# Kernel tuning notes

Measured on AMD Instinct MI355X. Metric: run time of the kernel, lower is better.

The kernel has to match this reference:

```python
import jax, jax.numpy as jnp
import numpy as np

N_NODES = 50000
N_EDGES = 800000
D_NODE = 64
D_EDGE = 64
MSG_DIM = 64           # n_features_list_messages[-1]
MLP_FEATS = [128, 128, 64]  # n_features_list_nodes
LN_EPS = 1e-6


def setup_inputs() -> dict:
    key = jax.random.key(0)
    ks = jax.random.split(key, 16)
    nodes = jax.random.normal(ks[0], (N_NODES, D_NODE), dtype=jnp.float32)
    edges = jax.random.normal(ks[1], (N_EDGES, D_EDGE), dtype=jnp.float32)
    senders = jax.random.randint(ks[2], (N_EDGES,), 0, N_NODES, dtype=jnp.int32)
    receivers = jax.random.randint(ks[3], (N_EDGES,), 0, N_NODES, dtype=jnp.int32)

    def glorot(k, shape):
        fan_in, fan_out = shape[0], shape[1]
        s = jnp.sqrt(2.0 / (fan_in + fan_out))
        return jax.random.normal(k, shape, dtype=jnp.float32) * s

    W_message = glorot(ks[4], (D_NODE + D_EDGE, MSG_DIM))      # no bias
    W_node = glorot(ks[5], (D_NODE, MLP_FEATS[-1]))            # no bias
    mlp_in_dim = D_NODE + MSG_DIM
    mlp_w0 = glorot(ks[6], (mlp_in_dim, MLP_FEATS[0]))
    mlp_b0 = jnp.zeros((MLP_FEATS[0],), dtype=jnp.float32)
    mlp_w1 = glorot(ks[7], (MLP_FEATS[0], MLP_FEATS[1]))
    mlp_b1 = jnp.zeros((MLP_FEATS[1],), dtype=jnp.float32)
    mlp_w2 = glorot(ks[8], (MLP_FEATS[1], MLP_FEATS[2]))
    mlp_b2 = jnp.zeros((MLP_FEATS[2],), dtype=jnp.float32)
    ln_scale = jnp.ones((MLP_FEATS[-1],), dtype=jnp.float32)
    ln_bias = jnp.zeros((MLP_FEATS[-1],), dtype=jnp.float32)

    return {
        "nodes": nodes, "edges": edges, "senders": senders, "receivers": receivers,
        "W_message": W_message, "W_node": W_node,
        "mlp_w0": mlp_w0, "mlp_b0": mlp_b0,
        "mlp_w1": mlp_w1, "mlp_b1": mlp_b1,
        "mlp_w2": mlp_w2, "mlp_b2": mlp_b2,
        "ln_scale": ln_scale, "ln_bias": ln_bias,
    }


def reference(nodes, edges, senders, receivers, W_message, W_node,
              mlp_w0, mlp_b0, mlp_w1, mlp_b1, mlp_w2, mlp_b2,
              ln_scale, ln_bias):
    # gather sender node features [E, d_node]
    sender_features = nodes[senders]
    # linear message on concat(sender, edge) [E, msg_dim]
    msg_in = jnp.concatenate([sender_features, edges], axis=-1)
    messages = msg_in @ W_message
    # scatter-add into receiver buckets [N, msg_dim]
    aggregated = jax.ops.segment_sum(messages, receivers, num_segments=N_NODES)
    # node MLP with ReLU hidden layers, linear output
    h = jnp.concatenate([nodes, aggregated], axis=-1)
    h = jax.nn.relu(h @ mlp_w0 + mlp_b0)
    h = jax.nn.relu(h @ mlp_w1 + mlp_b1)
    nodes_out = h @ mlp_w2 + mlp_b2
    # residual (linear skip) + LayerNorm
    x = nodes @ W_node + nodes_out
    mu = jnp.mean(x, axis=-1, keepdims=True)
    var = jnp.var(x, axis=-1, keepdims=True)
    nodes_new = (x - mu) * jax.lax.rsqrt(var + LN_EPS) * ln_scale + ln_bias
    return nodes_new
```

## Files before the change

### kernel.cpp

```cpp
#include <hip/hip_runtime.h>
#include <cstdint>
#include <cstddef>


__global__ void hist_k(const int* __restrict__ recv, int* __restrict__ hist, int E){
  int i = blockIdx.x*blockDim.x + threadIdx.x;
  if (i < E) atomicAdd(&hist[recv[i]], 1);
}

__global__ void s1_k(const int* __restrict__ hist, int* __restrict__ partial, int Nn){
  __shared__ int sh[256];
  int t = threadIdx.x;
  int i = blockIdx.x*256 + t;
  sh[t] = (i < Nn) ? hist[i] : 0;
  __syncthreads();
  for (int off = 128; off > 0; off >>= 1){
    if (t < off) sh[t] += sh[t + off];
    __syncthreads();
  }
  if (t == 0) partial[blockIdx.x] = sh[0];
}

__global__ void s2_k(int* __restrict__ partial, int nb){
  int lane = threadIdx.x;
  int run = 0;
  for (int base = 0; base < nb; base += 64){
    int v = (base + lane < nb) ? partial[base + lane] : 0;
    int x = v;
    #pragma unroll
    for (int off = 1; off < 64; off <<= 1){
      int y = __shfl_up(x, off);
      if (lane >= off) x += y;
    }
    if (base + lane < nb) partial[base + lane] = x - v + run;
    run += __shfl(x, 63);
  }
}

__global__ void s3_k(const int* __restrict__ hist, const int* __restrict__ partial,
                     int* __restrict__ offsets, int* __restrict__ cursor, int Nn){
  __shared__ int sh[256];
  int t = threadIdx.x;
  int i = blockIdx.x*256 + t;
  int v = (i < Nn) ? hist[i] : 0;
  sh[t] = v;
  __syncthreads();
  for (int off = 1; off < 256; off <<= 1){
    int x = (t >= off) ? sh[t - off] : 0;
    __syncthreads();
    sh[t] += x;
    __syncthreads();
  }
  if (i < Nn){
    int excl = sh[t] - v + partial[blockIdx.x];
    offsets[i] = excl;
    cursor[i]  = excl;
  }
}

__global__ void fill_k(const int* __restrict__ recv, const int* __restrict__ senders,
                       int* __restrict__ cursor, int2* __restrict__ csr_pack, int E){
  int i = blockIdx.x*blockDim.x + threadIdx.x;
  if (i < E){
    int r = recv[i];
    int s = senders[i];
    int pos = atomicAdd(&cursor[r], 1);
    csr_pack[pos] = make_int2(i, s);
  }
}

__global__ __launch_bounds__(256) void gather_sum_k(
    const float* __restrict__ nodes, const float* __restrict__ edges,
    const int2* __restrict__ csr_pack, const int* __restrict__ offsets,
    const int* __restrict__ hist, float* __restrict__ SE, int Nn)
{
  int wid  = threadIdx.x >> 6;
  int lane = threadIdx.x & 63;
  int node = blockIdx.x*4 + wid;
  if (node >= Nn) return;
  int start = offsets[node];
  int cnt   = hist[node];
  float sa = 0.f, ea = 0.f;
  int done = 0;
  while (done < cnt){
    int m = cnt - done; if (m > 64) m = 64;
    int2 pk = make_int2(0, 0);
    if (lane < m) pk = csr_pack[start + done + lane];
    int u = 0;
    for (; u + 4 <= m; u += 4){
      int e0 = __shfl(pk.x, u+0), s0 = __shfl(pk.y, u+0);
      int e1 = __shfl(pk.x, u+1), s1 = __shfl(pk.y, u+1);
      int e2 = __shfl(pk.x, u+2), s2 = __shfl(pk.y, u+2);
      int e3 = __shfl(pk.x, u+3), s3 = __shfl(pk.y, u+3);
      float n0 = nodes[(size_t)s0*64 + lane];
      float n1 = nodes[(size_t)s1*64 + lane];
      float n2 = nodes[(size_t)s2*64 + lane];
      float n3 = nodes[(size_t)s3*64 + lane];
      float g0 = edges[(size_t)e0*64 + lane];
      float g1 = edges[(size_t)e1*64 + lane];
      float g2 = edges[(size_t)e2*64 + lane];
      float g3 = edges[(size_t)e3*64 + lane];
      sa += (n0 + n1) + (n2 + n3);
      ea += (g0 + g1) + (g2 + g3);
    }
    for (; u < m; u++){
      int e0 = __shfl(pk.x, u), s0 = __shfl(pk.y, u);
      sa += nodes[(size_t)s0*64 + lane];
      ea += edges[(size_t)e0*64 + lane];
    }
    done += m;
  }
  SE[(size_t)node*128 + lane]      = sa;
  SE[(size_t)node*128 + 64 + lane] = ea;
}

__global__ void transpose_k(const float* __restrict__ in, float* __restrict__ out, int R, int C){
  __shared__ float tile[32][33];
  int c0 = blockIdx.x*32, r0 = blockIdx.y*32;
  int tx = threadIdx.x, ty = threadIdx.y;
  #pragma unroll
  for (int i = 0; i < 32; i += 8){
    int r = r0 + ty + i, c = c0 + tx;
    if (r < R && c < C) tile[ty + i][tx] = in[(size_t)r*C + c];
  }
  __syncthreads();
  #pragma unroll
  for (int i = 0; i < 32; i += 8){
    int c = c0 + ty + i, r = r0 + tx;
    if (r < R && c < C) out[(size_t)c*R + r] = tile[tx][ty + i];
  }
}

__global__ void wprep_k(const float* __restrict__ Wmsg, const float* __restrict__ w0,
                        const float* __restrict__ w2, const float* __restrict__ Wnode,
                        float* __restrict__ W1eff, float* __restrict__ W3eff){
  int idx = blockIdx.x*blockDim.x + threadIdx.x;
  if (idx < 192*128){
    int r = idx >> 7, j = idx & 127;
    float v;
    if (r < 64) v = w0[r*128 + j];
    else {
      int kk = r - 64;
      float a = 0.f;
      for (int m = 0; m < 64; m++) a = fmaf(Wmsg[kk*64 + m], w0[(64 + m)*128 + j], a);
      v = a;
    }
    W1eff[idx] = v;
  }
  if (idx < 192*64){
    int r = idx >> 6, j = idx & 63;
    W3eff[idx] = (r < 128) ? w2[r*64 + j] : Wnode[(r - 128)*64 + j];
  }
}


__global__ __launch_bounds__(256) void layer1_k(
    const float* __restrict__ nodesT, const float* __restrict__ SET,
    const float* __restrict__ W, const float* __restrict__ bias,
    float* __restrict__ outT, int N)
{
  int n  = blockIdx.x*256 + threadIdx.x;
  int jb = blockIdx.y*64;
  if (n >= N) return;
  float acc[64];
  #pragma unroll
  for (int j = 0; j < 64; j++) acc[j] = bias[jb + j];
  for (int k = 0; k < 64; k++){
    float x = nodesT[(size_t)k*N + n];
    #pragma unroll
    for (int j = 0; j < 64; j++) acc[j] = fmaf(x, W[k*128 + jb + j], acc[j]);
  }
  for (int k = 0; k < 128; k++){
    float x = SET[(size_t)k*N + n];
    #pragma unroll
    for (int j = 0; j < 64; j++) acc[j] = fmaf(x, W[(64 + k)*128 + jb + j], acc[j]);
  }
  #pragma unroll
  for (int j = 0; j < 64; j++) outT[(size_t)(jb + j)*N + n] = fmaxf(acc[j], 0.f);
}

__global__ __launch_bounds__(256) void layer2_k(
    const float* __restrict__ inT, const float* __restrict__ W, const float* __restrict__ bias,
    float* __restrict__ outT, int N)
{
  int n  = blockIdx.x*256 + threadIdx.x;
  int jb = blockIdx.y*64;
  if (n >= N) return;
  float acc[64];
  #pragma unroll
  for (int j = 0; j < 64; j++) acc[j] = bias[jb + j];
  for (int k = 0; k < 128; k++){
    float x = inT[(size_t)k*N + n];
    #pragma unroll
    for (int j = 0; j < 64; j++) acc[j] = fmaf(x, W[k*128 + jb + j], acc[j]);
  }
  #pragma unroll
  for (int j = 0; j < 64; j++) outT[(size_t)(jb + j)*N + n] = fmaxf(acc[j], 0.f);
}

__global__ __launch_bounds__(256) void layer3_k(
    const float* __restrict__ X2T, const float* __restrict__ nodesT,
    const float* __restrict__ W, const float* __restrict__ bias,
    const float* __restrict__ ln_scale, const float* __restrict__ ln_bias,
    float* __restrict__ out, int N)
{
  int n = blockIdx.x*256 + threadIdx.x;
  if (n >= N) return;
  float acc[64];
  #pragma unroll
  for (int j = 0; j < 64; j++) acc[j] = bias[j];
  for (int k = 0; k < 128; k++){
    float x = X2T[(size_t)k*N + n];
    #pragma unroll
    for (int j = 0; j < 64; j++) acc[j] = fmaf(x, W[k*64 + j], acc[j]);
  }
  for (int k = 0; k < 64; k++){
    float x = nodesT[(size_t)k*N + n];
    #pragma unroll
    for (int j = 0; j < 64; j++) acc[j] = fmaf(x, W[(128 + k)*64 + j], acc[j]);
  }
  float mu = 0.f;
  #pragma unroll
  for (int j = 0; j < 64; j++) mu += acc[j];
  mu *= (1.f/64.f);
  float var = 0.f;
  #pragma unroll
  for (int j = 0; j < 64; j++){ float d = acc[j] - mu; var = fmaf(d, d, var); }
  var *= (1.f/64.f);
  float inv = rsqrtf(var + 1e-6f);
  float4* o = (float4*)(out + (size_t)n*64);
  #pragma unroll
  for (int q = 0; q < 16; q++){
    float y0 = (acc[4*q+0] - mu)*inv*ln_scale[4*q+0] + ln_bias[4*q+0];
    float y1 = (acc[4*q+1] - mu)*inv*ln_scale[4*q+1] + ln_bias[4*q+1];
    float y2 = (acc[4*q+2] - mu)*inv*ln_scale[4*q+2] + ln_bias[4*q+2];
    float y3 = (acc[4*q+3] - mu)*inv*ln_scale[4*q+3] + ln_bias[4*q+3];
    o[q] = make_float4(y0, y1, y2, y3);
  }
}


extern "C" void kernel_launch(void* const* d_in, const int* in_sizes, int n_in,
                              void* d_out, int out_size, void* d_ws, size_t ws_size,
                              hipStream_t stream)
{
  const float* nodes   = (const float*)d_in[0];
  const float* edges   = (const float*)d_in[1];
  const int*   senders = (const int*)d_in[2];
  const int*   recv    = (const int*)d_in[3];
  const float* Wmsg    = (const float*)d_in[4];
  const float* Wnode   = (const float*)d_in[5];
  const float* w0      = (const float*)d_in[6];
  const float* b0      = (const float*)d_in[7];
  const float* w1      = (const float*)d_in[8];
  const float* b1      = (const float*)d_in[9];
  const float* w2      = (const float*)d_in[10];
  const float* b2      = (const float*)d_in[11];
  const float* lns     = (const float*)d_in[12];
  const float* lnb     = (const float*)d_in[13];
  float* out = (float*)d_out;

  const int N = in_sizes[0] / 64;
  const int E = in_sizes[2];

  auto align256 = [](size_t x){ return (x + 255) & ~(size_t)255; };
  char* p = (char*)d_ws;
  int* hist    = (int*)p; p += align256((size_t)N*4);
  int* offsets = (int*)p; p += align256((size_t)N*4);
  int* cursor  = (int*)p; p += align256((size_t)N*4);
  int* partial = (int*)p; p += align256(1024);
  int2* csr_pack = (int2*)p; p += align256((size_t)E*8);
  float* W1eff = (float*)p; p += align256((size_t)192*128*4);
  float* W3eff = (float*)p; p += align256((size_t)192*64*4);
  float* nodesT= (float*)p; p += align256((size_t)64*N*4);
  float* bufA  = (float*)p; p += align256((size_t)128*N*4);
  float* bufB  = (float*)p; p += align256((size_t)128*N*4);

  hipMemsetAsync(hist, 0, (size_t)N*4, stream);

  const int gridE = (E + 255)/256;
  const int nb    = (N + 255)/256;

  hist_k<<<gridE, 256, 0, stream>>>(recv, hist, E);
  s1_k<<<nb, 256, 0, stream>>>(hist, partial, N);
  s2_k<<<1, 64, 0, stream>>>(partial, nb);
  s3_k<<<nb, 256, 0, stream>>>(hist, partial, offsets, cursor, N);
  fill_k<<<gridE, 256, 0, stream>>>(recv, senders, cursor, csr_pack, E);

  gather_sum_k<<<(N + 3)/4, 256, 0, stream>>>(nodes, edges, csr_pack, offsets, hist, bufA, N);

  dim3 tb(32, 8);
  transpose_k<<<dim3(2, (N + 31)/32), tb, 0, stream>>>(nodes, nodesT, N, 64);
  transpose_k<<<dim3(4, (N + 31)/32), tb, 0, stream>>>(bufA, bufB, N, 128);

  wprep_k<<<(192*128 + 255)/256, 256, 0, stream>>>(Wmsg, w0, w2, Wnode, W1eff, W3eff);

  layer1_k<<<dim3(nb, 2), 256, 0, stream>>>(nodesT, bufB, W1eff, b0, bufA, N);
  layer2_k<<<dim3(nb, 2), 256, 0, stream>>>(bufA, w1, b1, bufB, N);
  layer3_k<<<nb, 256, 0, stream>>>(bufB, nodesT, W3eff, b2, lns, lnb, out, N);
}
```

Before: 644.4 us.

## Fuse transpose into gather, merge weight prep into scan, narrow MLP column tiles

Measured after the change: 673.6 us. 1.05x slower.

```diff
diff --git a/kernel.cpp b/kernel.cpp
--- a/kernel.cpp
+++ b/kernel.cpp
@@ -8,7 +8,10 @@
   if (i < E) atomicAdd(&hist[recv[i]], 1);
 }
 
-__global__ void s1_k(const int* __restrict__ hist, int* __restrict__ partial, int Nn){
+__global__ void s1_k(const int* __restrict__ hist, int* __restrict__ partial, int Nn,
+                     const float* __restrict__ Wmsg, const float* __restrict__ w0,
+                     const float* __restrict__ w2, const float* __restrict__ Wnode,
+                     float* __restrict__ W1eff, float* __restrict__ W3eff){
   __shared__ int sh[256];
   int t = threadIdx.x;
   int i = blockIdx.x*256 + t;
@@ -19,6 +22,24 @@
     __syncthreads();
   }
   if (t == 0) partial[blockIdx.x] = sh[0];
+
+  int idx = blockIdx.x*256 + t;
+  if (idx < 192*128){
+    int r = idx >> 7, j = idx & 127;
+    float v;
+    if (r < 64) v = w0[r*128 + j];
+    else {
+      int kk = r - 64;
+      float a = 0.f;
+      for (int m = 0; m < 64; m++) a = fmaf(Wmsg[kk*64 + m], w0[(64 + m)*128 + j], a);
+      v = a;
+    }
+    W1eff[idx] = v;
+  }
+  if (idx < 192*64){
+    int r = idx >> 6, j = idx & 63;
+    W3eff[idx] = (r < 128) ? w2[r*64 + j] : Wnode[(r - 128)*64 + j];
+  }
 }
 
 __global__ void s2_k(int* __restrict__ partial, int nb){
@@ -72,111 +93,97 @@
 __global__ __launch_bounds__(256) void gather_sum_k(
     const float* __restrict__ nodes, const float* __restrict__ edges,
     const int2* __restrict__ csr_pack, const int* __restrict__ offsets,
-    const int* __restrict__ hist, float* __restrict__ SE, int Nn)
-{
+    const int* __restrict__ hist, float* __restrict__ XT, int Nn)
+{
+  __shared__ float tile[128][65];
   int wid  = threadIdx.x >> 6;
   int lane = threadIdx.x & 63;
-  int node = blockIdx.x*4 + wid;
-  if (node >= Nn) return;
-  int start = offsets[node];
-  int cnt   = hist[node];
-  float sa = 0.f, ea = 0.f;
-  int done = 0;
-  while (done < cnt){
-    int m = cnt - done; if (m > 64) m = 64;
-    int2 pk = make_int2(0, 0);
-    if (lane < m) pk = csr_pack[start + done + lane];
-    int u = 0;
-    for (; u + 4 <= m; u += 4){
-      int e0 = __shfl(pk.x, u+0), s0 = __shfl(pk.y, u+0);
-      int e1 = __shfl(pk.x, u+1), s1 = __shfl(pk.y, u+1);
-      int e2 = __shfl(pk.x, u+2), s2 = __shfl(pk.y, u+2);
-      int e3 = __shfl(pk.x, u+3), s3 = __shfl(pk.y, u+3);
-      float n0 = nodes[(size_t)s0*64 + lane];
-      float n1 = nodes[(size_t)s1*64 + lane];
-      float n2 = nodes[(size_t)s2*64 + lane];
-      float n3 = nodes[(size_t)s3*64 + lane];
-      float g0 = edges[(size_t)e0*64 + lane];
-      float g1 = edges[(size_t)e1*64 + lane];
-      float g2 = edges[(size_t)e2*64 + lane];
-      float g3 = edges[(size_t)e3*64 + lane];
-      sa += (n0 + n1) + (n2 + n3);
-      ea += (g0 + g1) + (g2 + g3);
+  int nblock = blockIdx.x * 64;
+
+  for (int it = 0; it < 16; ++it){
+    int nd = nblock + wid*16 + it;
+    float sa = 0.f, ea = 0.f;
+    if (nd < Nn){
+      int start = offsets[nd];
+      int cnt   = hist[nd];
+      int done = 0;
+      while (done < cnt){
+        int m = cnt - done; if (m > 64) m = 64;
+        int2 pk = make_int2(0, 0);
+        if (lane < m) pk = csr_pack[start + done + lane];
+        int u = 0;
+        for (; u + 4 <= m; u += 4){
+          int e0 = __shfl(pk.x, u+0), s0 = __shfl(pk.y, u+0);
+          int e1 = __shfl(pk.x, u+1), s1 = __shfl(pk.y, u+1);
+          int e2 = __shfl(pk.x, u+2), s2 = __shfl(pk.y, u+2);
+          int e3 = __shfl(pk.x, u+3), s3 = __shfl(pk.y, u+3);
+          float n0 = nodes[(size_t)s0*64 + lane];
+          float n1 = nodes[(size_t)s1*64 + lane];
+          float n2 = nodes[(size_t)s2*64 + lane];
+          float n3 = nodes[(size_t)s3*64 + lane];
+          float g0 = edges[(size_t)e0*64 + lane];
+          float g1 = edges[(size_t)e1*64 + lane];
+          float g2 = edges[(size_t)e2*64 + lane];
+          float g3 = edges[(size_t)e3*64 + lane];
+          sa += (n0 + n1) + (n2 + n3);
+          ea += (g0 + g1) + (g2 + g3);
+        }
+        for (; u < m; u++){
+          int e0 = __shfl(pk.x, u), s0 = __shfl(pk.y, u);
+          sa += nodes[(size_t)s0*64 + lane];
+          ea += edges[(size_t)e0*64 + lane];
+        }
+        done += m;
+      }
     }
-    for (; u < m; u++){
-      int e0 = __shfl(pk.x, u), s0 = __shfl(pk.y, u);
-      sa += nodes[(size_t)s0*64 + lane];
-      ea += edges[(size_t)e0*64 + lane];
-    }
-    done += m;
-  }
-  SE[(size_t)node*128 + lane]      = sa;
-  SE[(size_t)node*128 + 64 + lane] = ea;
+    int c = wid*16 + it;
+    tile[lane][c]      = sa;
+    tile[64 + lane][c] = ea;
+  }
+  __syncthreads();
+
+  for (int r4 = 0; r4 < 128; r4 += 4){
+    int r = r4 + wid;
+    int n = nblock + lane;
+    if (n < Nn) XT[(size_t)(64 + r)*Nn + n] = tile[r][lane];
+  }
 }
 
 __global__ void transpose_k(const float* __restrict__ in, float* __restrict__ out, int R, int C){
-  __shared__ float tile[32][33];
+  __shared__ float tl[32][33];
   int c0 = blockIdx.x*32, r0 = blockIdx.y*32;
   int tx = threadIdx.x, ty = threadIdx.y;
   #pragma unroll
   for (int i = 0; i < 32; i += 8){
     int r = r0 + ty + i, c = c0 + tx;
-    if (r < R && c < C) tile[ty + i][tx] = in[(size_t)r*C + c];
+    if (r < R && c < C) tl[ty + i][tx] = in[(size_t)r*C + c];
   }
   __syncthreads();
   #pragma unroll
   for (int i = 0; i < 32; i += 8){
     int c = c0 + ty + i, r = r0 + tx;
-    if (r < R && c < C) out[(size_t)c*R + r] = tile[tx][ty + i];
-  }
-}
-
-__global__ void wprep_k(const float* __restrict__ Wmsg, const float* __restrict__ w0,
-                        const float* __restrict__ w2, const float* __restrict__ Wnode,
-                        float* __restrict__ W1eff, float* __restrict__ W3eff){
-  int idx = blockIdx.x*blockDim.x + threadIdx.x;
-  if (idx < 192*128){
-    int r = idx >> 7, j = idx & 127;
-    float v;
-    if (r < 64) v = w0[r*128 + j];
-    else {
-      int kk = r - 64;
-      float a = 0.f;
-      for (int m = 0; m < 64; m++) a = fmaf(Wmsg[kk*64 + m], w0[(64 + m)*128 + j], a);
-      v = a;
-    }
-    W1eff[idx] = v;
-  }
-  if (idx < 192*64){
-    int r = idx >> 6, j = idx & 63;
-    W3eff[idx] = (r < 128) ? w2[r*64 + j] : Wnode[(r - 128)*64 + j];
+    if (r < R && c < C) out[(size_t)c*R + r] = tl[tx][ty + i];
   }
 }
 
 
 __global__ __launch_bounds__(256) void layer1_k(
-    const float* __restrict__ nodesT, const float* __restrict__ SET,
-    const float* __restrict__ W, const float* __restrict__ bias,
+    const float* __restrict__ XT, const float* __restrict__ W, const float* __restrict__ bias,
     float* __restrict__ outT, int N)
 {
   int n  = blockIdx.x*256 + threadIdx.x;
-  int jb = blockIdx.y*64;
+  int jb = blockIdx.y*32;
   if (n >= N) return;
-  float acc[64];
-  #pragma unroll
-  for (int j = 0; j < 64; j++) acc[j] = bias[jb + j];
-  for (int k = 0; k < 64; k++){
-    float x = nodesT[(size_t)k*N + n];
-    #pragma unroll
-    for (int j = 0; j < 64; j++) acc[j] = fmaf(x, W[k*128 + jb + j], acc[j]);
-  }
-  for (int k = 0; k < 128; k++){
-    float x = SET[(size_t)k*N + n];
-    #pragma unroll
-    for (int j = 0; j < 64; j++) acc[j] = fmaf(x, W[(64 + k)*128 + jb + j], acc[j]);
-  }
-  #pragma unroll
-  for (int j = 0; j < 64; j++) outT[(size_t)(jb + j)*N + n] = fmaxf(acc[j], 0.f);
+  float acc[32];
+  #pragma unroll
+  for (int j = 0; j < 32; j++) acc[j] = bias[jb + j];
+  for (int k = 0; k < 192; k++){
+    float x = XT[(size_t)k*N + n];
+    #pragma unroll
+    for (int j = 0; j < 32; j++) acc[j] = fmaf(x, W[k*128 + jb + j], acc[j]);
+  }
+  #pragma unroll
+  for (int j = 0; j < 32; j++) outT[(size_t)(jb + j)*N + n] = fmaxf(acc[j], 0.f);
 }
 
 __global__ __launch_bounds__(256) void layer2_k(
@@ -184,18 +191,18 @@
     float* __restrict__ outT, int N)
 {
   int n  = blockIdx.x*256 + threadIdx.x;
-  int jb = blockIdx.y*64;
+  int jb = blockIdx.y*32;
   if (n >= N) return;
-  float acc[64];
-  #pragma unroll
-  for (int j = 0; j < 64; j++) acc[j] = bias[jb + j];
+  float acc[32];
+  #pragma unroll
+  for (int j = 0; j < 32; j++) acc[j] = bias[jb + j];
   for (int k = 0; k < 128; k++){
     float x = inT[(size_t)k*N + n];
     #pragma unroll
-    for (int j = 0; j < 64; j++) acc[j] = fmaf(x, W[k*128 + jb + j], acc[j]);
-  }
-  #pragma unroll
-  for (int j = 0; j < 64; j++) outT[(size_t)(jb + j)*N + n] = fmaxf(acc[j], 0.f);
+    for (int j = 0; j < 32; j++) acc[j] = fmaf(x, W[k*128 + jb + j], acc[j]);
+  }
+  #pragma unroll
+  for (int j = 0; j < 32; j++) outT[(size_t)(jb + j)*N + n] = fmaxf(acc[j], 0.f);
 }
 
 __global__ __launch_bounds__(256) void layer3_k(
@@ -272,7 +279,7 @@
   int2* csr_pack = (int2*)p; p += align256((size_t)E*8);
   float* W1eff = (float*)p; p += align256((size_t)192*128*4);
   float* W3eff = (float*)p; p += align256((size_t)192*64*4);
-  float* nodesT= (float*)p; p += align256((size_t)64*N*4);
+  float* XT    = (float*)p; p += align256((size_t)192*N*4);
   float* bufA  = (float*)p; p += align256((size_t)128*N*4);
   float* bufB  = (float*)p; p += align256((size_t)128*N*4);
 
@@ -282,20 +289,17 @@
   const int nb    = (N + 255)/256;
 
   hist_k<<<gridE, 256, 0, stream>>>(recv, hist, E);
-  s1_k<<<nb, 256, 0, stream>>>(hist, partial, N);
+  s1_k<<<nb, 256, 0, stream>>>(hist, partial, N, Wmsg, w0, w2, Wnode, W1eff, W3eff);
   s2_k<<<1, 64, 0, stream>>>(partial, nb);
   s3_k<<<nb, 256, 0, stream>>>(hist, partial, offsets, cursor, N);
   fill_k<<<gridE, 256, 0, stream>>>(recv, senders, cursor, csr_pack, E);
 
-  gather_sum_k<<<(N + 3)/4, 256, 0, stream>>>(nodes, edges, csr_pack, offsets, hist, bufA, N);
-
   dim3 tb(32, 8);
-  transpose_k<<<dim3(2, (N + 31)/32), tb, 0, stream>>>(nodes, nodesT, N, 64);
-  transpose_k<<<dim3(4, (N + 31)/32), tb, 0, stream>>>(bufA, bufB, N, 128);
-
-  wprep_k<<<(192*128 + 255)/256, 256, 0, stream>>>(Wmsg, w0, w2, Wnode, W1eff, W3eff);
-
-  layer1_k<<<dim3(nb, 2), 256, 0, stream>>>(nodesT, bufB, W1eff, b0, bufA, N);
-  layer2_k<<<dim3(nb, 2), 256, 0, stream>>>(bufA, w1, b1, bufB, N);
-  layer3_k<<<nb, 256, 0, stream>>>(bufB, nodesT, W3eff, b2, lns, lnb, out, N);
-}
+  transpose_k<<<dim3(2, (N + 31)/32), tb, 0, stream>>>(nodes, XT, N, 64);
+
+  gather_sum_k<<<(N + 63)/64, 256, 0, stream>>>(nodes, edges, csr_pack, offsets, hist, XT, N);
+
+  layer1_k<<<dim3(nb, 4), 256, 0, stream>>>(XT, W1eff, b0, bufA, N);
+  layer2_k<<<dim3(nb, 4), 256, 0, stream>>>(bufA, w1, b1, bufB, N);
+  layer3_k<<<nb, 256, 0, stream>>>(bufB, XT, W3eff, b2, lns, lnb, out, N);
+}
```
